# Performance work log

Hardware: AMD Instinct MI355X
Metric: run time of the kernel (lower is better)

Reference implementation:

```python
import jax, jax.numpy as jnp
import numpy as np
import math

B, T, C, H = 4, 2048, 1024, 16
DH = C // H  # 64

def setup_inputs() -> dict:
    key = jax.random.key(0)
    k1, k2, k3 = jax.random.split(key, 3)
    x = jax.random.normal(k1, (B, T, C), dtype=jnp.float32)
    # standard RoPE angle table: [T, DH/2]
    inv_freq = 1.0 / (10000.0 ** (jnp.arange(0, DH, 2, dtype=jnp.float32) / DH))
    ang = jnp.arange(T, dtype=jnp.float32)[:, None] * inv_freq[None, :]
    cos = jnp.cos(ang)
    sin = jnp.sin(ang)
    Wqkv = jax.random.normal(k2, (3 * C, C), dtype=jnp.float32) * (C ** -0.5)
    Wo = jax.random.normal(k3, (C, C), dtype=jnp.float32) * (C ** -0.5)
    return {"x": x, "cos": cos, "sin": sin, "Wqkv": Wqkv, "Wo": Wo}

def apply_rotary(x, cos, sin):
    # x: [B,H,T,DH]; cos/sin: [T, DH/2] broadcast over B,H
    x1, x2 = x[..., ::2], x[..., 1::2]
    xr = jnp.stack([x1 * cos - x2 * sin, x1 * sin + x2 * cos], axis=-1)
    return xr.reshape(x.shape)

def reference(x, cos, sin, Wqkv, Wo):
    Bz, Tz, Cz = x.shape
    qkv = x @ Wqkv.T  # [B,T,3C]
    q, k, v = jnp.split(qkv, 3, axis=-1)
    def heads(t):
        return t.reshape(Bz, Tz, H, DH).transpose(0, 2, 1, 3)  # [B,H,T,DH]
    q, k, v = heads(q), heads(k), heads(v)
    q = apply_rotary(q, cos, sin)
    k = apply_rotary(k, cos, sin)
    attn = jnp.einsum('bhqd,bhkd->bhqk', q, k) / math.sqrt(DH)
    causal = jnp.tril(jnp.ones((Tz, Tz), dtype=bool))
    attn = jnp.where(causal, attn, jnp.float32(-jnp.inf))
    attn = jax.nn.softmax(attn, axis=-1)
    y = jnp.einsum('bhqk,bhkd->bhqd', attn, v)
    y = y.transpose(0, 2, 1, 3).reshape(Bz, Tz, Cz)
    return y @ Wo.T
```

## Files before the change

kernel.cpp:

```cpp
#include <hip/hip_runtime.h>
#include <math.h>

#define Bz 4
#define Tz 2048
#define Cz 1024
#define Hz 16
#define DHz 64
#define Mz (Bz*Tz)

typedef __attribute__((ext_vector_type(8))) short short8;
typedef __attribute__((ext_vector_type(4))) float f32x4;
typedef __attribute__((ext_vector_type(2))) float flt2;
typedef __attribute__((ext_vector_type(4))) float flt4;
typedef unsigned long long u64;

__device__ inline unsigned short f2bf(float f){
  union { float f; unsigned int u; } x; x.f = f;
  unsigned int r = x.u + 0x7fffu + ((x.u >> 16) & 1u);
  return (unsigned short)(r >> 16);
}
__device__ inline float bf2f(unsigned short b){
  union { unsigned int u; float f; } x; x.u = ((unsigned int)b) << 16; return x.f;
}
__device__ inline unsigned int packbf2(float lo, float hi){
  union { float f; unsigned int u; } a, b; a.f = lo; b.f = hi;
  return __builtin_amdgcn_perm(b.u, a.u, 0x07060302u);
}
__device__ inline u64 pack4bf(float a, float b, float c, float d){
  return (u64)f2bf(a) | ((u64)f2bf(b) << 16) | ((u64)f2bf(c) << 32) | ((u64)f2bf(d) << 48);
}

__device__ inline void gload_lds16(const unsigned short* g, char* l){
  __builtin_amdgcn_global_load_lds((const __attribute__((address_space(1))) unsigned int*)g,
                                   (__attribute__((address_space(3))) unsigned int*)l,
                                   16, 0, 0);
}

#define NXE 8388608
#define NW1 3145728
__global__ __launch_bounds__(256) void cvt_all(const float* __restrict__ x,
                                               const float* __restrict__ wq,
                                               const float* __restrict__ wo,
                                               unsigned short* __restrict__ xb,
                                               unsigned short* __restrict__ wqb,
                                               unsigned short* __restrict__ wob){
  int i = (blockIdx.x * 256 + threadIdx.x) * 4;
  const float* s; unsigned short* d;
  if (i < NXE){ s = x + i; d = xb + i; }
  else if (i < NXE + NW1){ s = wq + (i - NXE); d = wqb + (i - NXE); }
  else { s = wo + (i - NXE - NW1); d = wob + (i - NXE - NW1); }
  flt4 v = *(const flt4*)s;
  *(u64*)d = pack4bf(v.x, v.y, v.z, v.w);
}

template<int SWAP>
__device__ __forceinline__ void gemm_core(const unsigned short* __restrict__ As0,
                                          const unsigned short* __restrict__ Bs0,
                                          char* At, char* Bt,
                                          int tid, int wid, int l16, int lg, int wr, int wc,
                                          f32x4 acc[4][4])
{
  const int srow = tid >> 3;
  const int scol = (tid & 7) ^ (srow & 7);
  for (int kt = 0; kt < 16; ++kt){
    const unsigned short* As = As0 + kt * 64;
    const unsigned short* Bs = Bs0 + kt * 64;
    #pragma unroll
    for (int it = 0; it < 4; ++it){
      gload_lds16(As + (size_t)(it * 32 + srow) * 1024 + scol * 8, At + it * 4096 + wid * 1024);
      gload_lds16(Bs + (size_t)(it * 32 + srow) * 1024 + scol * 8, Bt + it * 4096 + wid * 1024);
    }
    __syncthreads();
    #pragma unroll
    for (int ks = 0; ks < 2; ++ks){
      short8 af[4], bf[4];
      #pragma unroll
      for (int mt = 0; mt < 4; ++mt){
        int row = wr * 64 + mt * 16 + l16;
        af[mt] = *(const short8*)(At + row * 128 + (((ks * 4 + lg) ^ (row & 7)) << 4));
      }
      #pragma unroll
      for (int nt = 0; nt < 4; ++nt){
        int row = wc * 64 + nt * 16 + l16;
        bf[nt] = *(const short8*)(Bt + row * 128 + (((ks * 4 + lg) ^ (row & 7)) << 4));
      }
      #pragma unroll
      for (int mt = 0; mt < 4; ++mt)
        #pragma unroll
        for (int nt = 0; nt < 4; ++nt)
          acc[mt][nt] = SWAP
            ? __builtin_amdgcn_mfma_f32_16x16x32_bf16(bf[nt], af[mt], acc[mt][nt], 0, 0, 0)
            : __builtin_amdgcn_mfma_f32_16x16x32_bf16(af[mt], bf[nt], acc[mt][nt], 0, 0, 0);
    }
    __syncthreads();
  }
}

__global__ __launch_bounds__(256)
void gemm_qkv(const unsigned short* __restrict__ A, const unsigned short* __restrict__ Bw,
              unsigned short* __restrict__ qd, unsigned short* __restrict__ kd,
              unsigned short* __restrict__ vd,
              const float* __restrict__ cosb, const float* __restrict__ sinb)
{
  __shared__ __align__(16) char lds[32768];
  char* At = lds; char* Bt = lds + 16384;

  const int swz = (blockIdx.x & 7) * 192 + (blockIdx.x >> 3);
  const int nb = swz % 24, mb = swz / 24;
  const int m0 = mb * 128, n0 = nb * 128;

  const int tid  = threadIdx.x;
  const int lane = tid & 63, wid = tid >> 6;
  const int l16  = lane & 15, lg = lane >> 4;
  const int wr   = wid >> 1, wc = wid & 1;
  const int part = n0 >> 10;

  f32x4 acc[4][4] = {};

  if (part < 2){
    gemm_core<1>(A + (size_t)m0 * 1024, Bw + (size_t)n0 * 1024, At, Bt,
                 tid, wid, l16, lg, wr, wc, acc);
    unsigned short* dst = part ? kd : qd;
    const float qs = part ? 1.0f : 0.125f * 1.4426950408889634f;
    #pragma unroll
    for (int mt = 0; mt < 4; ++mt){
      int m = m0 + wr * 64 + mt * 16 + l16;
      int b = m >> 11, t = m & 2047;
      const float* cb = cosb + t * 32;
      const float* sb = sinb + t * 32;
      #pragma unroll
      for (int nt = 0; nt < 4; ++nt){
        int n4 = (n0 & 1023) + wc * 64 + nt * 16 + lg * 4;
        int h = n4 >> 6, d0 = n4 & 63;
        flt2 c = *(const flt2*)(cb + (d0 >> 1));
        flt2 s = *(const flt2*)(sb + (d0 >> 1));
        float x0 = acc[mt][nt][0], x1 = acc[mt][nt][1];
        float x2 = acc[mt][nt][2], x3 = acc[mt][nt][3];
        float r0 = (x0 * c.x - x1 * s.x) * qs;
        float r1 = (x0 * s.x + x1 * c.x) * qs;
        float r2 = (x2 * c.y - x3 * s.y) * qs;
        float r3 = (x2 * s.y + x3 * c.y) * qs;
        *(u64*)(dst + (((size_t)(b * Hz + h)) * Tz + t) * DHz + d0) = pack4bf(r0, r1, r2, r3);
      }
    }
  } else {
    gemm_core<0>(A + (size_t)m0 * 1024, Bw + (size_t)n0 * 1024, At, Bt,
                 tid, wid, l16, lg, wr, wc, acc);
    #pragma unroll
    for (int mt = 0; mt < 4; ++mt)
      #pragma unroll
      for (int nt = 0; nt < 4; ++nt){
        int m = m0 + wr * 64 + mt * 16 + lg * 4;
        int n = (n0 & 1023) + wc * 64 + nt * 16 + l16;
        int h = n >> 6, d = n & 63;
        int b = m >> 11, t = m & 2047;
        *(u64*)(vd + (((size_t)(b * Hz + h)) * DHz + d) * Tz + t)
          = pack4bf(acc[mt][nt][0], acc[mt][nt][1], acc[mt][nt][2], acc[mt][nt][3]);
      }
  }
}

__global__ __launch_bounds__(256)
void gemm_out(const unsigned short* __restrict__ A, const unsigned short* __restrict__ Bw,
              float* __restrict__ outf)
{
  __shared__ __align__(16) char lds[32768];
  char* At = lds; char* Bt = lds + 16384;

  const int swz = (blockIdx.x & 7) * 64 + (blockIdx.x >> 3);
  const int nb = swz % 8, mb = swz / 8;
  const int m0 = mb * 128, n0 = nb * 128;

  const int tid  = threadIdx.x;
  const int lane = tid & 63, wid = tid >> 6;
  const int l16  = lane & 15, lg = lane >> 4;
  const int wr   = wid >> 1, wc = wid & 1;

  f32x4 acc[4][4] = {};
  gemm_core<1>(A + (size_t)m0 * 1024, Bw + (size_t)n0 * 1024, At, Bt,
               tid, wid, l16, lg, wr, wc, acc);

  #pragma unroll
  for (int mt = 0; mt < 4; ++mt){
    int m = m0 + wr * 64 + mt * 16 + l16;
    #pragma unroll
    for (int nt = 0; nt < 4; ++nt){
      int n = n0 + wc * 64 + nt * 16 + lg * 4;
      *(f32x4*)(outf + (size_t)m * 1024 + n) = acc[mt][nt];
    }
  }
}

__global__ __launch_bounds__(256)
void attn_fwd(const unsigned short* __restrict__ qh, const unsigned short* __restrict__ kh,
              const unsigned short* __restrict__ vt, unsigned short* __restrict__ y)
{
  __shared__ __align__(16) char lds[40960];
  const int tid  = threadIdx.x;
  const int lane = tid & 63, wid = tid >> 6;
  const int l16  = lane & 15, lg = lane >> 4;
  const int swzb = (blockIdx.x & 7) * 256 + (blockIdx.x >> 3);
  const int bh   = swzb >> 5;
  const int qt   = 31 - (swzb & 31);

  const size_t base = (size_t)bh * Tz * DHz;
  const unsigned short* qb = qh + base;
  const unsigned short* kb = kh + base;
  const unsigned short* vb = vt + base;

  const int qrow = qt * 64 + wid * 16 + l16;
  short8 qf[2];
  qf[0] = *(const short8*)(qb + (size_t)qrow * DHz + 0  + lg * 8);
  qf[1] = *(const short8*)(qb + (size_t)qrow * DHz + 32 + lg * 8);

  const int x07 = l16 & 7;
  const int fo0 = l16 * 128 + (((0 + lg) ^ x07) << 4);
  const int fo1 = l16 * 128 + (((4 + lg) ^ x07) << 4);
  char* const Pb = (char*)lds + 32768 + wid * 2048;
  int pw[4], prd[2];
  #pragma unroll
  for (int nt = 0; nt < 4; ++nt)
    pw[nt] = l16 * 128 + ((((nt << 1) + (lg >> 1)) ^ x07) << 4) + ((lg & 1) << 3);
  prd[0] = l16 * 128 + (((0 + lg) ^ x07) << 4);
  prd[1] = l16 * 128 + (((4 + lg) ^ x07) << 4);

  const int srow = tid >> 3;
  const int scol = (tid & 7) ^ (srow & 7);
  const int kOff = srow * DHz + scol * 8;
  const size_t vOff = (size_t)srow * Tz + scol * 8;

  auto STAGE = [&](int kt, int c){
    const unsigned short* Ks = kb + (size_t)kt * 64 * DHz;
    const unsigned short* Vs = vb + kt * 64;
    char* KD = (char*)lds + c * 8192;
    char* VD = (char*)lds + 16384 + c * 8192;
    #pragma unroll
    for (int it = 0; it < 2; ++it){
      gload_lds16(Ks + kOff + it * 32 * DHz, KD + it * 4096 + wid * 1024);
      gload_lds16(Vs + vOff + (size_t)it * 32 * Tz, VD + it * 4096 + wid * 1024);
    }
  };

  short8 ones;
  #pragma unroll
  for (int j = 0; j < 8; ++j) ones[j] = (short)0x3F80;

  f32x4 o[4] = {};
  f32x4 lsum = {};
  float m_r = -INFINITY;

  auto TILE = [&](bool diag, int kt, const char* KL, const char* VL){
    f32x4 s[4] = {};
    __builtin_amdgcn_s_setprio(1);
    #pragma unroll
    for (int nt = 0; nt < 4; ++nt){
      short8 kf = *(const short8*)(KL + fo0 + nt * 2048);
      s[nt] = __builtin_amdgcn_mfma_f32_16x16x32_bf16(kf, qf[0], s[nt], 0, 0, 0);
    }
    #pragma unroll
    for (int nt = 0; nt < 4; ++nt){
      short8 kf = *(const short8*)(KL + fo1 + nt * 2048);
      s[nt] = __builtin_amdgcn_mfma_f32_16x16x32_bf16(kf, qf[1], s[nt], 0, 0, 0);
    }
    __builtin_amdgcn_s_setprio(0);

    if (diag){
      #pragma unroll
      for (int nt = 0; nt < 4; ++nt)
        #pragma unroll
        for (int r = 0; r < 4; ++r){
          int kv = kt * 64 + nt * 16 + lg * 4 + r;
          if (kv > qrow) s[nt][r] = -INFINITY;
        }
    }

    float mx = fmaxf(fmaxf(fmaxf(fmaxf(s[0][0], s[0][1]), fmaxf(s[0][2], s[0][3])),
                           fmaxf(fmaxf(s[1][0], s[1][1]), fmaxf(s[1][2], s[1][3]))),
                     fmaxf(fmaxf(fmaxf(s[2][0], s[2][1]), fmaxf(s[2][2], s[2][3])),
                           fmaxf(fmaxf(s[3][0], s[3][1]), fmaxf(s[3][2], s[3][3]))));
    mx = fmaxf(mx, __shfl_xor(mx, 16));
    mx = fmaxf(mx, __shfl_xor(mx, 32));

    if (!__all(mx - m_r <= 8.0f)){
      float mn = fmaxf(m_r, mx);
      float al = __builtin_amdgcn_exp2f(m_r - mn);
      #pragma unroll
      for (int nt = 0; nt < 4; ++nt)
        #pragma unroll
        for (int i = 0; i < 4; ++i) o[nt][i] *= al;
      #pragma unroll
      for (int i = 0; i < 4; ++i) lsum[i] *= al;
      m_r = mn;
    }

    #pragma unroll
    for (int nt = 0; nt < 4; ++nt){
      float p0 = __builtin_amdgcn_exp2f(s[nt][0] - m_r);
      float p1 = __builtin_amdgcn_exp2f(s[nt][1] - m_r);
      float p2 = __builtin_amdgcn_exp2f(s[nt][2] - m_r);
      float p3 = __builtin_amdgcn_exp2f(s[nt][3] - m_r);
      *(u64*)(Pb + pw[nt]) = (u64)packbf2(p0, p1) | ((u64)packbf2(p2, p3) << 32);
    }

    __builtin_amdgcn_s_setprio(1);
    #pragma unroll
    for (int ks = 0; ks < 2; ++ks){
      short8 pa = *(const short8*)(Pb + prd[ks]);
      lsum = __builtin_amdgcn_mfma_f32_16x16x32_bf16(ones, pa, lsum, 0, 0, 0);
      const int fo = ks ? fo1 : fo0;
      #pragma unroll
      for (int nt = 0; nt < 4; ++nt){
        short8 vf = *(const short8*)(VL + fo + nt * 2048);
        o[nt] = __builtin_amdgcn_mfma_f32_16x16x32_bf16(vf, pa, o[nt], 0, 0, 0);
      }
    }
    __builtin_amdgcn_s_setprio(0);
  };

  int cur = 0;
  STAGE(0, 0);
  __syncthreads();

  for (int kt = 0; kt < qt; ++kt){
    STAGE(kt + 1, cur ^ 1);
    TILE(false, kt, (const char*)lds + cur * 8192, (const char*)lds + 16384 + cur * 8192);
    __syncthreads();
    cur ^= 1;
  }
  TILE(true, qt, (const char*)lds + cur * 8192, (const char*)lds + 16384 + cur * 8192);

  const int b = bh >> 4, h = bh & 15;
  const int row = qt * 64 + wid * 16 + l16;
  unsigned short* yb = y + ((size_t)b * Tz + row) * Cz + h * 64 + lg * 4;
  float inv = 1.f / lsum[0];
  #pragma unroll
  for (int nt = 0; nt < 4; ++nt)
    *(u64*)(yb + nt * 16) = pack4bf(o[nt][0] * inv, o[nt][1] * inv,
                                    o[nt][2] * inv, o[nt][3] * inv);
}

extern "C" void kernel_launch(void* const* d_in, const int* in_sizes, int n_in,
                              void* d_out, int out_size, void* d_ws, size_t ws_size,
                              hipStream_t stream)
{
  const float* x    = (const float*)d_in[0];
  const float* cosb = (const float*)d_in[1];
  const float* sinb = (const float*)d_in[2];
  const float* Wqkv = (const float*)d_in[3];
  const float* Wo   = (const float*)d_in[4];
  float* out = (float*)d_out;

  char* ws = (char*)d_ws;
  unsigned short* xb    = (unsigned short*)(ws);
  unsigned short* ybuf  = xb;
  unsigned short* wqkvb = (unsigned short*)(ws + 16777216);
  unsigned short* wob   = (unsigned short*)(ws + 23068672);
  unsigned short* qhb   = (unsigned short*)(ws + 25165824);
  unsigned short* khb   = (unsigned short*)(ws + 41943040);
  unsigned short* vtb   = (unsigned short*)(ws + 58720256);

  cvt_all<<<12288, 256, 0, stream>>>(x, Wqkv, Wo, xb, wqkvb, wob);

  gemm_qkv<<<1536, 256, 0, stream>>>(xb, wqkvb, qhb, khb, vtb, cosb, sinb);

  attn_fwd<<<2048, 256, 0, stream>>>(qhb, khb, vtb, ybuf);

  gemm_out<<<512, 256, 0, stream>>>(ybuf, wob, out);
}
```

Baseline: 273.0 us.

## Use 128-row query tiles with 8 waves in attention and 2D launch grids

The attention kernel now handles 128 query rows per block with 512 threads (8 waves). Each staged 64-key K/V tile is shared by twice as many query rows, which halves the global K/V traffic per query and lets every thread issue a single load per stage. Causal masking now applies to the last two key tiles. The GEMM and attention launches move from 1D grids with XCD/L2 swizzling to plain 2D grids, which drops the swizzle arithmetic but may reduce cache locality. Larger blocks also lower occupancy and add more masked work on the diagonal.

```diff
diff --git a/kernel.cpp b/kernel.cpp
--- a/kernel.cpp
+++ b/kernel.cpp
@@ -105,8 +105,7 @@
   __shared__ __align__(16) char lds[32768];
   char* At = lds; char* Bt = lds + 16384;
 
-  const int swz = (blockIdx.x & 7) * 192 + (blockIdx.x >> 3);
-  const int nb = swz % 24, mb = swz / 24;
+  const int nb = blockIdx.x, mb = blockIdx.y;
   const int m0 = mb * 128, n0 = nb * 128;
 
   const int tid  = threadIdx.x;
@@ -167,8 +166,7 @@
   __shared__ __align__(16) char lds[32768];
   char* At = lds; char* Bt = lds + 16384;
 
-  const int swz = (blockIdx.x & 7) * 64 + (blockIdx.x >> 3);
-  const int nb = swz % 8, mb = swz / 8;
+  const int nb = blockIdx.x, mb = blockIdx.y;
   const int m0 = mb * 128, n0 = nb * 128;
 
   const int tid  = threadIdx.x;
@@ -191,24 +189,24 @@
   }
 }
 
-__global__ __launch_bounds__(256)
+__global__ __launch_bounds__(512)
 void attn_fwd(const unsigned short* __restrict__ qh, const unsigned short* __restrict__ kh,
               const unsigned short* __restrict__ vt, unsigned short* __restrict__ y)
 {
-  __shared__ __align__(16) char lds[40960];
+  __shared__ __align__(16) char lds[49152];
   const int tid  = threadIdx.x;
   const int lane = tid & 63, wid = tid >> 6;
   const int l16  = lane & 15, lg = lane >> 4;
-  const int swzb = (blockIdx.x & 7) * 256 + (blockIdx.x >> 3);
-  const int bh   = swzb >> 5;
-  const int qt   = 31 - (swzb & 31);
+  const int bh   = blockIdx.x;
+  const int qt   = 15 - blockIdx.y;
+  const int q0   = qt * 128;
 
   const size_t base = (size_t)bh * Tz * DHz;
   const unsigned short* qb = qh + base;
   const unsigned short* kb = kh + base;
   const unsigned short* vb = vt + base;
 
-  const int qrow = qt * 64 + wid * 16 + l16;
+  const int qrow = q0 + wid * 16 + l16;
   short8 qf[2];
   qf[0] = *(const short8*)(qb + (size_t)qrow * DHz + 0  + lg * 8);
   qf[1] = *(const short8*)(qb + (size_t)qrow * DHz + 32 + lg * 8);
@@ -221,8 +219,7 @@
   #pragma unroll
   for (int nt = 0; nt < 4; ++nt)
     pw[nt] = l16 * 128 + ((((nt << 1) + (lg >> 1)) ^ x07) << 4) + ((lg & 1) << 3);
-  prd[0] = l16 * 128 + (((0 + lg) ^ x07) << 4);
-  prd[1] = l16 * 128 + (((4 + lg) ^ x07) << 4);
+  prd[0] = fo0; prd[1] = fo1;
 
   const int srow = tid >> 3;
   const int scol = (tid & 7) ^ (srow & 7);
@@ -230,15 +227,8 @@
   const size_t vOff = (size_t)srow * Tz + scol * 8;
 
   auto STAGE = [&](int kt, int c){
-    const unsigned short* Ks = kb + (size_t)kt * 64 * DHz;
-    const unsigned short* Vs = vb + kt * 64;
-    char* KD = (char*)lds + c * 8192;
-    char* VD = (char*)lds + 16384 + c * 8192;
-    #pragma unroll
-    for (int it = 0; it < 2; ++it){
-      gload_lds16(Ks + kOff + it * 32 * DHz, KD + it * 4096 + wid * 1024);
-      gload_lds16(Vs + vOff + (size_t)it * 32 * Tz, VD + it * 4096 + wid * 1024);
-    }
+    gload_lds16(kb + (size_t)kt * 64 * DHz + kOff, (char*)lds + c * 8192 + tid * 16);
+    gload_lds16(vb + (size_t)kt * 64 + vOff, (char*)lds + 16384 + c * 8192 + tid * 16);
   };
 
   short8 ones;
@@ -321,17 +311,19 @@
   STAGE(0, 0);
   __syncthreads();
 
-  for (int kt = 0; kt < qt; ++kt){
+  const int last = 2 * qt + 1;
+  for (int kt = 0; kt < last; ++kt){
     STAGE(kt + 1, cur ^ 1);
-    TILE(false, kt, (const char*)lds + cur * 8192, (const char*)lds + 16384 + cur * 8192);
+    TILE(kt >= 2 * qt, kt, (const char*)lds + cur * 8192,
+         (const char*)lds + 16384 + cur * 8192);
     __syncthreads();
     cur ^= 1;
   }
-  TILE(true, qt, (const char*)lds + cur * 8192, (const char*)lds + 16384 + cur * 8192);
+  TILE(true, last, (const char*)lds + cur * 8192,
+       (const char*)lds + 16384 + cur * 8192);
 
   const int b = bh >> 4, h = bh & 15;
-  const int row = qt * 64 + wid * 16 + l16;
-  unsigned short* yb = y + ((size_t)b * Tz + row) * Cz + h * 64 + lg * 4;
+  unsigned short* yb = y + ((size_t)b * Tz + qrow) * Cz + h * 64 + lg * 4;
   float inv = 1.f / lsum[0];
   #pragma unroll
   for (int nt = 0; nt < 4; ++nt)
@@ -361,9 +353,9 @@
 
   cvt_all<<<12288, 256, 0, stream>>>(x, Wqkv, Wo, xb, wqkvb, wob);
 
-  gemm_qkv<<<1536, 256, 0, stream>>>(xb, wqkvb, qhb, khb, vtb, cosb, sinb);
-
-  attn_fwd<<<2048, 256, 0, stream>>>(qhb, khb, vtb, ybuf);
-
-  gemm_out<<<512, 256, 0, stream>>>(ybuf, wob, out);
-}
+  gemm_qkv<<<dim3(24, 64), 256, 0, stream>>>(xb, wqkvb, qhb, khb, vtb, cosb, sinb);
+
+  attn_fwd<<<dim3(64, 16), 512, 0, stream>>>(qhb, khb, vtb, ybuf);
+
+  gemm_out<<<dim3(8, 64), 256, 0, stream>>>(ybuf, wob, out);
+}
```

Measured after the change: 262.2 us. -3.9%, faster.
